# Kernel optimization log

Measured on AMD Instinct MI355X. Metric: run time of the kernel, lower is better.

The kernel has to match this reference:

```python
import jax, jax.numpy as jnp
import numpy as np

NEG_INF = -1e9


def setup_inputs() -> dict:
    key = jax.random.key(0)
    k1, k2, k3, k4 = jax.random.split(key, 4)
    N, F_in, F_out = 8192, 512, 256
    features = jax.random.normal(k1, (N, F_in), dtype=jnp.float32)
    adj = jax.random.randint(k2, (N, N), 0, 2).astype(jnp.float32)
    W = jax.random.normal(k3, (F_in, F_out), dtype=jnp.float32) * 0.05
    a = jax.random.normal(k4, (2 * F_out,), dtype=jnp.float32) * 0.05
    return {"features": features, "adj": adj, "W": W, "a": a}


def reference(features, adj, W, a):
    # h = W @ features  -> [N, F_out]
    h = features @ W
    F_out = h.shape[1]
    a_src, a_dst = a[:F_out], a[F_out:]
    # a^T [h_i ; h_j] decomposes into per-node dot products (same math as
    # the concat+linear in the original, without the [N,N,2F] intermediate).
    e = jax.nn.leaky_relu((h @ a_src)[:, None] + (h @ a_dst)[None, :],
                          negative_slope=0.01)  # [N, N]
    masked_e = e + NEG_INF * (1.0 - adj)
    attention = jax.nn.softmax(masked_e, axis=1)  # row-wise over neighbors j
    output = attention @ h  # [N, F_out]
    return output, attention
```

## Files before the change

### kernel.cpp

```cpp
#include <hip/hip_runtime.h>
#include <hip/hip_bf16.h>

#define N 8192
#define FIN 512
#define FOUT 256

typedef __attribute__((ext_vector_type(8))) short bf16x8;
typedef __attribute__((ext_vector_type(4))) float f32x4;

__device__ __forceinline__ unsigned short f2bf(float x) {
  unsigned int u = __float_as_uint(x);
  return (unsigned short)((u + 0x7FFFu + ((u >> 16) & 1u)) >> 16);
}

__global__ __launch_bounds__(256) void gat_k1_gemm_h(
    const float* __restrict__ A, const float* __restrict__ W,
    float* __restrict__ h, unsigned short* __restrict__ hT) {
  __shared__ __align__(16) float As[16][68];
  __shared__ __align__(16) float Bs[16][64];
  const int tid = threadIdx.x;
  const int tx = tid & 15, ty = tid >> 4;
  const int nb = blockIdx.x * 64, mb = blockIdx.y * 64;
  float acc[4][4] = {};
  for (int k0 = 0; k0 < FIN; k0 += 16) {
#pragma unroll
    for (int i = 0; i < 4; ++i) {
      int e = tid + 256 * i;
      int m = e >> 4, k = e & 15;
      As[k][m] = A[(size_t)(mb + m) * FIN + k0 + k];
      int n2 = e & 63, k2 = e >> 6;
      Bs[k2][n2] = W[(size_t)(k0 + k2) * FOUT + nb + n2];
    }
    __syncthreads();
#pragma unroll
    for (int k = 0; k < 16; ++k) {
      float4 av = *reinterpret_cast<const float4*>(&As[k][ty * 4]);
      float4 bv = *reinterpret_cast<const float4*>(&Bs[k][tx * 4]);
      float aa[4] = {av.x, av.y, av.z, av.w};
      float bb[4] = {bv.x, bv.y, bv.z, bv.w};
#pragma unroll
      for (int i = 0; i < 4; ++i)
#pragma unroll
        for (int j = 0; j < 4; ++j) acc[i][j] = fmaf(aa[i], bb[j], acc[i][j]);
    }
    __syncthreads();
  }
#pragma unroll
  for (int i = 0; i < 4; ++i) {
    int m = mb + ty * 4 + i;
#pragma unroll
    for (int j = 0; j < 4; ++j) {
      int n = nb + tx * 4 + j;
      h[(size_t)m * FOUT + n] = acc[i][j];
      hT[(size_t)n * N + m] = f2bf(acc[i][j]);
    }
  }
}

__global__ __launch_bounds__(256) void gat_k2_hshd(
    const float* __restrict__ h, const float* __restrict__ a,
    float* __restrict__ hs, float* __restrict__ hd, float* __restrict__ out) {
  const int gid = blockIdx.x * 256 + threadIdx.x;
  *reinterpret_cast<float4*>(out + (size_t)gid * 4) =
      make_float4(0.f, 0.f, 0.f, 0.f);

  const int wid = threadIdx.x >> 6;
  const int lane = threadIdx.x & 63;
  const int row = blockIdx.x * 4 + wid;
  float ps = 0.f, pd = 0.f;
#pragma unroll
  for (int i = 0; i < 4; ++i) {
    int c = lane + 64 * i;
    float v = h[(size_t)row * FOUT + c];
    ps += v * a[c];
    pd += v * a[FOUT + c];
  }
#pragma unroll
  for (int off = 32; off >= 1; off >>= 1) {
    ps += __shfl_down(ps, off);
    pd += __shfl_down(pd, off);
  }
  if (lane == 0) {
    hs[row] = ps;
    hd[row] = pd;
  }
}

__global__ __launch_bounds__(256) void gat_k3_attn(
    const float* __restrict__ adj, const float* __restrict__ hs,
    const float* __restrict__ hd, float* __restrict__ att) {
  __shared__ __align__(16) float hd_s[N];
  __shared__ float red[4];
  const int tid = threadIdx.x;
  const int lane = tid & 63, wid = tid >> 6;
#pragma unroll
  for (int i = 0; i < 8; ++i) {
    int j = tid * 4 + 1024 * i;
    *reinterpret_cast<float4*>(&hd_s[j]) =
        *reinterpret_cast<const float4*>(&hd[j]);
  }
  __syncthreads();
  const int row0 = blockIdx.x * 8;
  for (int r = 0; r < 8; ++r) {
    const int row = row0 + r;
    const float hsv = hs[row];
    const float* arow = adj + (size_t)row * N;
    float4 l[8];
    float m = -__builtin_inff();
#pragma unroll
    for (int i = 0; i < 8; ++i) {
      int j = tid * 4 + 1024 * i;
      float4 a4 = *reinterpret_cast<const float4*>(&arow[j]);
      float4 h4 = *reinterpret_cast<const float4*>(&hd_s[j]);
      float4 lv;
      float x;
      x = hsv + h4.x; x = x > 0.f ? x : 0.01f * x;
      lv.x = (a4.x != 0.f) ? x : -__builtin_inff();
      x = hsv + h4.y; x = x > 0.f ? x : 0.01f * x;
      lv.y = (a4.y != 0.f) ? x : -__builtin_inff();
      x = hsv + h4.z; x = x > 0.f ? x : 0.01f * x;
      lv.z = (a4.z != 0.f) ? x : -__builtin_inff();
      x = hsv + h4.w; x = x > 0.f ? x : 0.01f * x;
      lv.w = (a4.w != 0.f) ? x : -__builtin_inff();
      l[i] = lv;
      m = fmaxf(m, fmaxf(fmaxf(lv.x, lv.y), fmaxf(lv.z, lv.w)));
    }
#pragma unroll
    for (int off = 32; off >= 1; off >>= 1) m = fmaxf(m, __shfl_down(m, off));
    if (lane == 0) red[wid] = m;
    __syncthreads();
    m = fmaxf(fmaxf(red[0], red[1]), fmaxf(red[2], red[3]));
    __syncthreads();
    float s = 0.f;
#pragma unroll
    for (int i = 0; i < 8; ++i) {
      float4 lv = l[i];
      lv.x = __expf(lv.x - m);
      lv.y = __expf(lv.y - m);
      lv.z = __expf(lv.z - m);
      lv.w = __expf(lv.w - m);
      l[i] = lv;
      s += lv.x + lv.y + lv.z + lv.w;
    }
#pragma unroll
    for (int off = 32; off >= 1; off >>= 1) s += __shfl_down(s, off);
    if (lane == 0) red[wid] = s;
    __syncthreads();
    s = red[0] + red[1] + red[2] + red[3];
    __syncthreads();
    const float inv = 1.f / s;
    float* orow = att + (size_t)row * N;
#pragma unroll
    for (int i = 0; i < 8; ++i) {
      float4 lv = l[i];
      lv.x *= inv; lv.y *= inv; lv.z *= inv; lv.w *= inv;
      *reinterpret_cast<float4*>(&orow[tid * 4 + 1024 * i]) = lv;
    }
  }
}

__global__ __launch_bounds__(1024) void gat_k4_out(
    const float* __restrict__ att, const unsigned short* __restrict__ hT,
    float* __restrict__ C) {
  __shared__ __align__(16) unsigned short As[2][128 * 64];
  __shared__ __align__(16) unsigned short Bs[2][256 * 64];
  const int tid = threadIdx.x;
  const int lane = tid & 63;
  const int wid = tid >> 6;
  const int wm = wid >> 2, wn = wid & 3;
  const int g = lane >> 4, rsel = lane & 15;
  const int id = blockIdx.x;
  const int grp = id & 7, pos = id >> 3;
  const int kq = grp & 3;
  const int rb = (grp >> 2) + 2 * pos;
  const int row0 = rb * 128;
  const int kbase = kq * 2048;

  const float* asrc[2];
  int abyte[2];
#pragma unroll
  for (int i = 0; i < 2; ++i) {
    int e = tid + 1024 * i;
    int r = e >> 4, p = e & 15;
    asrc[i] = att + (size_t)(row0 + r) * N + kbase + p * 4;
    abyte[i] = r * 128 + ((p * 8) ^ ((r & 7) << 4));
  }
  const unsigned short* bsrc[2];
  int bbyte[2];
#pragma unroll
  for (int i = 0; i < 2; ++i) {
    int s = tid + 1024 * i;
    int n = s >> 3, kg = s & 7;
    int kgs = kg ^ (n & 7);
    bsrc[i] = hT + (size_t)n * N + kbase + kgs * 8;
    bbyte[i] = s * 16;
  }

  f32x4 acc[2][4] = {};
  float4 aA0, aA1;
  uint4 bB0, bB1;

  aA0 = *reinterpret_cast<const float4*>(asrc[0]);
  aA1 = *reinterpret_cast<const float4*>(asrc[1]);
  bB0 = *reinterpret_cast<const uint4*>(bsrc[0]);
  bB1 = *reinterpret_cast<const uint4*>(bsrc[1]);
  {
    uint2 pk;
    pk.x = (unsigned)f2bf(aA0.x) | ((unsigned)f2bf(aA0.y) << 16);
    pk.y = (unsigned)f2bf(aA0.z) | ((unsigned)f2bf(aA0.w) << 16);
    *reinterpret_cast<uint2*>(reinterpret_cast<char*>(As[0]) + abyte[0]) = pk;
    pk.x = (unsigned)f2bf(aA1.x) | ((unsigned)f2bf(aA1.y) << 16);
    pk.y = (unsigned)f2bf(aA1.z) | ((unsigned)f2bf(aA1.w) << 16);
    *reinterpret_cast<uint2*>(reinterpret_cast<char*>(As[0]) + abyte[1]) = pk;
    *reinterpret_cast<uint4*>(reinterpret_cast<char*>(Bs[0]) + bbyte[0]) = bB0;
    *reinterpret_cast<uint4*>(reinterpret_cast<char*>(Bs[0]) + bbyte[1]) = bB1;
  }

  int cur = 0;
  for (int t = 0; t < 32; ++t) {
    const int knext = (t + 1) * 64;
    if (t < 31) {
      aA0 = *reinterpret_cast<const float4*>(asrc[0] + knext);
      aA1 = *reinterpret_cast<const float4*>(asrc[1] + knext);
      bB0 = *reinterpret_cast<const uint4*>(bsrc[0] + knext);
      bB1 = *reinterpret_cast<const uint4*>(bsrc[1] + knext);
    }
    __syncthreads();
    const char* Ac = reinterpret_cast<const char*>(As[cur]);
    const char* Bc = reinterpret_cast<const char*>(Bs[cur]);
#pragma unroll
    for (int ks = 0; ks < 2; ++ks) {
      bf16x8 af[2], bg[4];
#pragma unroll
      for (int f = 0; f < 2; ++f) {
        int r = wm * 32 + f * 16 + rsel;
        af[f] = *reinterpret_cast<const bf16x8*>(
            Ac + r * 128 + ((ks * 64 + g * 16) ^ ((r & 7) << 4)));
      }
#pragma unroll
      for (int f = 0; f < 4; ++f) {
        int n = wn * 64 + f * 16 + rsel;
        bg[f] = *reinterpret_cast<const bf16x8*>(
            Bc + n * 128 + ((ks * 64 + g * 16) ^ ((n & 7) << 4)));
      }
#pragma unroll
      for (int i = 0; i < 2; ++i)
#pragma unroll
        for (int j = 0; j < 4; ++j)
          acc[i][j] = __builtin_amdgcn_mfma_f32_16x16x32_bf16(af[i], bg[j],
                                                              acc[i][j], 0, 0, 0);
    }
    if (t < 31) {
      char* An = reinterpret_cast<char*>(As[cur ^ 1]);
      char* Bn = reinterpret_cast<char*>(Bs[cur ^ 1]);
      uint2 pk;
      pk.x = (unsigned)f2bf(aA0.x) | ((unsigned)f2bf(aA0.y) << 16);
      pk.y = (unsigned)f2bf(aA0.z) | ((unsigned)f2bf(aA0.w) << 16);
      *reinterpret_cast<uint2*>(An + abyte[0]) = pk;
      pk.x = (unsigned)f2bf(aA1.x) | ((unsigned)f2bf(aA1.y) << 16);
      pk.y = (unsigned)f2bf(aA1.z) | ((unsigned)f2bf(aA1.w) << 16);
      *reinterpret_cast<uint2*>(An + abyte[1]) = pk;
      *reinterpret_cast<uint4*>(Bn + bbyte[0]) = bB0;
      *reinterpret_cast<uint4*>(Bn + bbyte[1]) = bB1;
      cur ^= 1;
    }
  }
#pragma unroll
  for (int i = 0; i < 2; ++i)
#pragma unroll
    for (int j = 0; j < 4; ++j)
#pragma unroll
      for (int r = 0; r < 4; ++r) {
        int row = row0 + wm * 32 + i * 16 + g * 4 + r;
        int col = wn * 64 + j * 16 + rsel;
        atomicAdd(&C[(size_t)row * FOUT + col], acc[i][j][r]);
      }
}

extern "C" void kernel_launch(void* const* d_in, const int* in_sizes, int n_in,
                              void* d_out, int out_size, void* d_ws, size_t ws_size,
                              hipStream_t stream) {
  const float* features = (const float*)d_in[0];
  const float* adj = (const float*)d_in[1];
  const float* W = (const float*)d_in[2];
  const float* a = (const float*)d_in[3];

  float* out = (float*)d_out;
  float* att = out + (size_t)N * FOUT;

  char* ws = (char*)d_ws;
  float* h = (float*)ws;
  unsigned short* hT = (unsigned short*)(ws + (size_t)N * FOUT * 4);
  float* hs = (float*)(ws + (size_t)N * FOUT * 4 + (size_t)N * FOUT * 2);
  float* hd = hs + N;

  hipLaunchKernelGGL(gat_k1_gemm_h, dim3(FOUT / 64, N / 64), dim3(256), 0,
                     stream, features, W, h, hT);
  hipLaunchKernelGGL(gat_k2_hshd, dim3(N / 4), dim3(256), 0, stream, h, a, hs,
                     hd, out);
  hipLaunchKernelGGL(gat_k3_attn, dim3(N / 8), dim3(256), 0, stream, adj, hs,
                     hd, att);
  hipLaunchKernelGGL(gat_k4_out, dim3(256), dim3(1024), 0, stream, att, hT,
                     out);
}
```

Measured before the change: 232.4 us.

## Retile output GEMM into 64x128 blocks with N-split and two-way K-split

Reworks the attention@h kernel to use 512-thread blocks computing 64-row by 128-column tiles, splitting the output columns in halves and K into two halves instead of quarters, with 512 blocks and two blocks per CU. The block-to-XCD mapping is changed so each XCD handles a fixed column half and K half. The aim is to raise occupancy and shrink shared memory per block so more blocks overlap latency. The cost is that each attention row tile is now read twice, once per column half, and the K loop per block is longer.

```diff
diff --git a/kernel.cpp b/kernel.cpp
--- a/kernel.cpp
+++ b/kernel.cpp
@@ -159,44 +159,44 @@
   }
 }
 
-__global__ __launch_bounds__(1024) void gat_k4_out(
+__global__ __launch_bounds__(512, 2) void gat_k4_out(
     const float* __restrict__ att, const unsigned short* __restrict__ hT,
     float* __restrict__ C) {
-  __shared__ __align__(16) unsigned short As[2][128 * 64];
-  __shared__ __align__(16) unsigned short Bs[2][256 * 64];
+  __shared__ __align__(16) unsigned short As[2][64 * 64];
+  __shared__ __align__(16) unsigned short Bs[2][128 * 64];
   const int tid = threadIdx.x;
   const int lane = tid & 63;
   const int wid = tid >> 6;
   const int wm = wid >> 2, wn = wid & 3;
   const int g = lane >> 4, rsel = lane & 15;
   const int id = blockIdx.x;
-  const int grp = id & 7, pos = id >> 3;
-  const int kq = grp & 3;
-  const int rb = (grp >> 2) + 2 * pos;
-  const int row0 = rb * 128;
-  const int kbase = kq * 2048;
+  const int xcd = id & 7, pos = id >> 3;
+  const int nh = xcd & 1, kh = (xcd >> 1) & 1;
+  const int row0 = ((xcd >> 2) * 64 + pos) * 64;
+  const int nb = nh * 128;
+  const int kbase = kh * 4096;
 
   const float* asrc[2];
   int abyte[2];
 #pragma unroll
   for (int i = 0; i < 2; ++i) {
-    int e = tid + 1024 * i;
+    int e = tid + 512 * i;
     int r = e >> 4, p = e & 15;
     asrc[i] = att + (size_t)(row0 + r) * N + kbase + p * 4;
     abyte[i] = r * 128 + ((p * 8) ^ ((r & 7) << 4));
   }
   const unsigned short* bsrc[2];
-  int bbyte[2];
+  int bofs[2];
 #pragma unroll
   for (int i = 0; i < 2; ++i) {
-    int s = tid + 1024 * i;
+    int s = tid + 512 * i;
     int n = s >> 3, kg = s & 7;
     int kgs = kg ^ (n & 7);
-    bsrc[i] = hT + (size_t)n * N + kbase + kgs * 8;
-    bbyte[i] = s * 16;
-  }
-
-  f32x4 acc[2][4] = {};
+    bsrc[i] = hT + (size_t)(nb + n) * N + kbase + kgs * 8;
+    bofs[i] = s * 16;
+  }
+
+  f32x4 acc[2][2] = {};
   float4 aA0, aA1;
   uint4 bB0, bB1;
 
@@ -212,14 +212,14 @@
     pk.x = (unsigned)f2bf(aA1.x) | ((unsigned)f2bf(aA1.y) << 16);
     pk.y = (unsigned)f2bf(aA1.z) | ((unsigned)f2bf(aA1.w) << 16);
     *reinterpret_cast<uint2*>(reinterpret_cast<char*>(As[0]) + abyte[1]) = pk;
-    *reinterpret_cast<uint4*>(reinterpret_cast<char*>(Bs[0]) + bbyte[0]) = bB0;
-    *reinterpret_cast<uint4*>(reinterpret_cast<char*>(Bs[0]) + bbyte[1]) = bB1;
+    *reinterpret_cast<uint4*>(reinterpret_cast<char*>(Bs[0]) + bofs[0]) = bB0;
+    *reinterpret_cast<uint4*>(reinterpret_cast<char*>(Bs[0]) + bofs[1]) = bB1;
   }
 
   int cur = 0;
-  for (int t = 0; t < 32; ++t) {
+  for (int t = 0; t < 64; ++t) {
     const int knext = (t + 1) * 64;
-    if (t < 31) {
+    if (t < 63) {
       aA0 = *reinterpret_cast<const float4*>(asrc[0] + knext);
       aA1 = *reinterpret_cast<const float4*>(asrc[1] + knext);
       bB0 = *reinterpret_cast<const uint4*>(bsrc[0] + knext);
@@ -230,27 +230,24 @@
     const char* Bc = reinterpret_cast<const char*>(Bs[cur]);
 #pragma unroll
     for (int ks = 0; ks < 2; ++ks) {
-      bf16x8 af[2], bg[4];
+      bf16x8 af[2], bg[2];
 #pragma unroll
       for (int f = 0; f < 2; ++f) {
         int r = wm * 32 + f * 16 + rsel;
         af[f] = *reinterpret_cast<const bf16x8*>(
             Ac + r * 128 + ((ks * 64 + g * 16) ^ ((r & 7) << 4)));
-      }
-#pragma unroll
-      for (int f = 0; f < 4; ++f) {
-        int n = wn * 64 + f * 16 + rsel;
+        int n = wn * 32 + f * 16 + rsel;
         bg[f] = *reinterpret_cast<const bf16x8*>(
             Bc + n * 128 + ((ks * 64 + g * 16) ^ ((n & 7) << 4)));
       }
 #pragma unroll
       for (int i = 0; i < 2; ++i)
 #pragma unroll
-        for (int j = 0; j < 4; ++j)
+        for (int j = 0; j < 2; ++j)
           acc[i][j] = __builtin_amdgcn_mfma_f32_16x16x32_bf16(af[i], bg[j],
                                                               acc[i][j], 0, 0, 0);
     }
-    if (t < 31) {
+    if (t < 63) {
       char* An = reinterpret_cast<char*>(As[cur ^ 1]);
       char* Bn = reinterpret_cast<char*>(Bs[cur ^ 1]);
       uint2 pk;
@@ -260,19 +257,19 @@
       pk.x = (unsigned)f2bf(aA1.x) | ((unsigned)f2bf(aA1.y) << 16);
       pk.y = (unsigned)f2bf(aA1.z) | ((unsigned)f2bf(aA1.w) << 16);
       *reinterpret_cast<uint2*>(An + abyte[1]) = pk;
-      *reinterpret_cast<uint4*>(Bn + bbyte[0]) = bB0;
-      *reinterpret_cast<uint4*>(Bn + bbyte[1]) = bB1;
+      *reinterpret_cast<uint4*>(Bn + bofs[0]) = bB0;
+      *reinterpret_cast<uint4*>(Bn + bofs[1]) = bB1;
       cur ^= 1;
     }
   }
 #pragma unroll
   for (int i = 0; i < 2; ++i)
 #pragma unroll
-    for (int j = 0; j < 4; ++j)
+    for (int j = 0; j < 2; ++j)
 #pragma unroll
       for (int r = 0; r < 4; ++r) {
         int row = row0 + wm * 32 + i * 16 + g * 4 + r;
-        int col = wn * 64 + j * 16 + rsel;
+        int col = nb + wn * 32 + j * 16 + rsel;
         atomicAdd(&C[(size_t)row * FOUT + col], acc[i][j][r]);
       }
 }
@@ -300,6 +297,6 @@
                      hd, out);
   hipLaunchKernelGGL(gat_k3_attn, dim3(N / 8), dim3(256), 0, stream, adj, hs,
                      hd, att);
-  hipLaunchKernelGGL(gat_k4_out, dim3(256), dim3(1024), 0, stream, att, hT,
+  hipLaunchKernelGGL(gat_k4_out, dim3(512), dim3(512), 0, stream, att, hT,
                      out);
 }
```

Result: slower. 250.7 us (+7.9%).
